# Kernel optimization log

Measured on AMD Instinct MI355X. Metric: run time of the kernel, lower is better.

The kernel has to match this reference:

```python
import jax, jax.numpy as jnp
import numpy as np

L, H, P = 16384, 1024, 512
DT_MIN, DT_MAX = 1e-3, 1e-1


def setup_inputs() -> dict:
    key = jax.random.key(0)
    ks = jax.random.split(key, 9)
    input_sequence = jax.random.normal(ks[0], (L, H), dtype=jnp.float32)
    # HiPPO-like diagonal init: negative real parts, spread imaginary parts
    Lambda_re = -0.5 * jnp.ones((P,), dtype=jnp.float32)
    Lambda_im = jnp.pi * jnp.arange(P, dtype=jnp.float32)
    # B_tilde = Vinv @ B with lecun_normal B -> ~N(0, 1/H) entries
    B_re = jax.random.normal(ks[1], (P, H), dtype=jnp.float32) / np.float32(np.sqrt(H))
    B_im = jax.random.normal(ks[2], (P, H), dtype=jnp.float32) / np.float32(np.sqrt(H))
    # C_tilde = C @ V, lecun_normal scale ~1/sqrt(2P)
    C_re = jax.random.normal(ks[3], (H, P), dtype=jnp.float32) / np.float32(np.sqrt(2 * P))
    C_im = jax.random.normal(ks[4], (H, P), dtype=jnp.float32) / np.float32(np.sqrt(2 * P))
    D = jax.random.normal(ks[5], (H,), dtype=jnp.float32)
    # log_step ~ U[log(dt_min), log(dt_max)], shape (P, 1)
    u01 = jax.random.uniform(ks[6], (P, 1), dtype=jnp.float32)
    log_step = jnp.log(DT_MIN) + u01 * (jnp.log(DT_MAX) - jnp.log(DT_MIN))
    return {
        "input_sequence": input_sequence,
        "Lambda_re": Lambda_re, "Lambda_im": Lambda_im,
        "B_re": B_re, "B_im": B_im,
        "C_re": C_re, "C_im": C_im,
        "D": D, "log_step": log_step,
    }


def _binop(q_i, q_j):
    # diagonal linear recurrence combine: x_j = A_j * x_i + b_j
    A_i, b_i = q_i
    A_j, b_j = q_j
    return (A_j * A_i, A_j * b_i + b_j)


def reference(input_sequence, Lambda_re, Lambda_im, B_re, B_im, C_re, C_im, D, log_step):
    # step_rescale = 1.0, clip_eigs = False, conj_sym = True, zoh discretization
    step = jnp.exp(log_step[:, 0])                      # (P,)
    Lam = Lambda_re + 1j * Lambda_im                    # (P,) complex64
    Lambda_bar = jnp.exp(Lam * step)                    # (P,)
    B_tilde = B_re + 1j * B_im                          # (P, H)
    B_bar = ((Lambda_bar - 1.0) / Lam)[:, None] * B_tilde  # (P, H)

    # bf16-split complex matvec: Bu_t = B_bar @ u_t (u real) for all t at once
    Bre_bf = jnp.real(B_bar).astype(jnp.bfloat16)
    Bim_bf = jnp.imag(B_bar).astype(jnp.bfloat16)
    u_bf = input_sequence.astype(jnp.bfloat16)          # (L, H)
    Bu_re = jnp.einsum('ph,lh->lp', Bre_bf, u_bf).astype(jnp.float32)
    Bu_im = jnp.einsum('ph,lh->lp', Bim_bf, u_bf).astype(jnp.float32)
    Bu = Bu_re + 1j * Bu_im                             # (L, P) complex64

    Lambda_elems = Lambda_bar * jnp.ones((input_sequence.shape[0], Lambda_bar.shape[0]),
                                         dtype=Lambda_bar.dtype)  # (L, P)
    _, xs = jax.lax.associative_scan(_binop, (Lambda_elems, Bu))  # xs: (L, P) complex64

    # bf16-split complex matvec y = C_tilde @ x, keep real part only
    Cre_bf = C_re.astype(jnp.bfloat16)
    Cim_bf = C_im.astype(jnp.bfloat16)
    xre_bf = jnp.real(xs).astype(jnp.bfloat16)
    xim_bf = jnp.imag(xs).astype(jnp.bfloat16)
    rr = jnp.einsum('hp,lp->lh', Cre_bf, xre_bf)
    ii = jnp.einsum('hp,lp->lh', Cim_bf, xim_bf)
    y_real = (rr - ii).astype(jnp.float32)              # (L, H)
    ys = 2.0 * y_real                                   # conj_sym doubling

    # feedthrough
    return ys + D * input_sequence
```

## Files before the change

### kernel.cpp

```cpp
#include <hip/hip_runtime.h>
#include <stdint.h>
#include <stddef.h>

#define L_SEQ 16384
#define H_DIM 1024
#define P_DIM 512
#define N2P   1024
#define CHUNK 64
#define NCH   256

typedef __bf16 bf16x8 __attribute__((ext_vector_type(8)));
typedef float  f32x4  __attribute__((ext_vector_type(4)));
typedef unsigned short u16x8 __attribute__((ext_vector_type(8)));

__device__ __forceinline__ unsigned short f2bf(float x) {
  unsigned int u = __float_as_uint(x);
  u += 0x7FFFu + ((u >> 16) & 1u);
  return (unsigned short)(u >> 16);
}
__device__ __forceinline__ float bf2f(unsigned short x) {
  return __uint_as_float((unsigned int)x << 16);
}

__global__ void k_prep_p(const float* __restrict__ Lre, const float* __restrict__ Lim,
                         const float* __restrict__ lstep,
                         float2* __restrict__ lam, double2* __restrict__ lamK,
                         float2* __restrict__ coeff) {
  int p = blockIdx.x * blockDim.x + threadIdx.x;
  if (p >= P_DIM) return;
  double step = exp((double)lstep[p]);
  double ar = (double)Lre[p] * step;
  double ai = (double)Lim[p] * step;
  double er = exp(ar);
  double lr = er * cos(ai), li = er * sin(ai);
  lam[p] = make_float2((float)lr, (float)li);
  double ka = (double)CHUNK * ai;
  double kr = exp((double)CHUNK * ar);
  lamK[p] = make_double2(kr * cos(ka), kr * sin(ka));
  double nr = lr - 1.0, ni = li;
  double dr = (double)Lre[p], di = (double)Lim[p];
  double den = dr * dr + di * di;
  coeff[p] = make_float2((float)((nr * dr + ni * di) / den),
                         (float)((ni * dr - nr * di) / den));
}

__global__ void k_pack_B(const float* __restrict__ Bre, const float* __restrict__ Bim,
                         const float2* __restrict__ coeff, unsigned short* __restrict__ Bp) {
  int idx = blockIdx.x * 256 + threadIdx.x;
  int p = idx >> 10, h = idx & 1023;
  float2 c = coeff[p];
  float br = Bre[idx], bi = Bim[idx];
  Bp[(size_t)(2 * p) * H_DIM + h]     = f2bf(c.x * br - c.y * bi);
  Bp[(size_t)(2 * p + 1) * H_DIM + h] = f2bf(c.x * bi + c.y * br);
}

__global__ void k_pack_C(const float* __restrict__ Cre, const float* __restrict__ Cim,
                         unsigned short* __restrict__ Cp) {
  int idx = blockIdx.x * 256 + threadIdx.x;
  int h = idx >> 10, j = idx & 1023;
  int p = j >> 1;
  float v = (j & 1) ? -Cim[(size_t)h * P_DIM + p] : Cre[(size_t)h * P_DIM + p];
  Cp[idx] = f2bf(v);
}

__global__ void k_cast_u(const float* __restrict__ U, unsigned short* __restrict__ Ub) {
  size_t base = ((size_t)blockIdx.x * 256 + threadIdx.x) * 8;
  const float4* s = (const float4*)(U + base);
  float4 v0 = s[0], v1 = s[1];
  u16x8 o;
  o[0] = f2bf(v0.x); o[1] = f2bf(v0.y); o[2] = f2bf(v0.z); o[3] = f2bf(v0.w);
  o[4] = f2bf(v1.x); o[5] = f2bf(v1.y); o[6] = f2bf(v1.z); o[7] = f2bf(v1.w);
  *(u16x8*)(Ub + base) = o;
}

template <int OUT>
__global__ void gemm_bt(const unsigned short* __restrict__ A,
                        const unsigned short* __restrict__ B,
                        void* __restrict__ Cout,
                        const unsigned short* __restrict__ Ub,
                        const float* __restrict__ Dv) {
  const int K = 1024, N = 1024;
  __shared__ unsigned short sA[128 * 64];
  __shared__ unsigned short sB[128 * 64];
  const int tid = threadIdx.x;
  const int wave = tid >> 6, lane = tid & 63;
  const int quad = lane >> 4, l16 = lane & 15;
  const int m0 = blockIdx.x * 128, n0 = blockIdx.y * 128;
  const int wm = (wave & 1) * 64, wn = (wave >> 1) * 64;

  f32x4 acc[4][4] = {};

  for (int kt = 0; kt < K; kt += 64) {
    __syncthreads();
#pragma unroll
    for (int r = 0; r < 4; ++r) {
      int id2 = r * 256 + tid;
      const unsigned short* ga = A + (size_t)(m0 + (id2 >> 3)) * K + kt + (id2 & 7) * 8;
      const unsigned short* gb = B + (size_t)(n0 + (id2 >> 3)) * K + kt + (id2 & 7) * 8;
      __builtin_amdgcn_global_load_lds(
          (const __attribute__((address_space(1))) unsigned int*)ga,
          (__attribute__((address_space(3))) unsigned int*)(sA + (r * 256 + wave * 64) * 8),
          16, 0, 0);
      __builtin_amdgcn_global_load_lds(
          (const __attribute__((address_space(1))) unsigned int*)gb,
          (__attribute__((address_space(3))) unsigned int*)(sB + (r * 256 + wave * 64) * 8),
          16, 0, 0);
    }
    __syncthreads();

#pragma unroll
    for (int h = 0; h < 2; ++h) {
      bf16x8 af[4], bfr[4];
#pragma unroll
      for (int i = 0; i < 4; ++i)
        af[i] = *(const bf16x8*)(sA + (wm + i * 16 + l16) * 64 + h * 32 + quad * 8);
#pragma unroll
      for (int j = 0; j < 4; ++j)
        bfr[j] = *(const bf16x8*)(sB + (wn + j * 16 + l16) * 64 + h * 32 + quad * 8);
#pragma unroll
      for (int i = 0; i < 4; ++i)
#pragma unroll
        for (int j = 0; j < 4; ++j)
          acc[i][j] = __builtin_amdgcn_mfma_f32_16x16x32_bf16(af[i], bfr[j], acc[i][j], 0, 0, 0);
    }
  }

#pragma unroll
  for (int i = 0; i < 4; ++i) {
#pragma unroll
    for (int j = 0; j < 4; ++j) {
      int col = n0 + wn + j * 16 + l16;
#pragma unroll
      for (int r = 0; r < 4; ++r) {
        int row = m0 + wm + i * 16 + quad * 4 + r;
        size_t o = (size_t)row * N + col;
        float v = acc[i][j][r];
        if (OUT) {
          float u = bf2f(Ub[o]);
          ((float*)Cout)[o] = 2.0f * v + Dv[col] * u;
        } else {
          ((unsigned short*)Cout)[o] = f2bf(v);
        }
      }
    }
  }
}

__global__ void k_scanA(const unsigned short* __restrict__ Bu, const float2* __restrict__ lam,
                        float2* __restrict__ csum) {
  int idx = blockIdx.x * 256 + threadIdx.x;
  int p = idx & (P_DIM - 1), chunk = idx >> 9;
  float2 l = lam[p];
  float xr = 0.f, xi = 0.f;
  const unsigned int* base = (const unsigned int*)(Bu + (size_t)chunk * CHUNK * N2P + 2 * p);
#pragma unroll 8
  for (int t = 0; t < CHUNK; ++t) {
    unsigned int v = base[(size_t)t * (N2P / 2)];
    float br = bf2f((unsigned short)(v & 0xffffu));
    float bi = bf2f((unsigned short)(v >> 16));
    float nr = fmaf(l.x, xr, fmaf(-l.y, xi, br));
    float ni = fmaf(l.x, xi, fmaf(l.y, xr, bi));
    xr = nr; xi = ni;
  }
  csum[(size_t)chunk * P_DIM + p] = make_float2(xr, xi);
}

__global__ void k_scanB(const float2* __restrict__ csum, const double2* __restrict__ lamK,
                        float2* __restrict__ carry) {
  int p = blockIdx.x * 256 + threadIdx.x;
  if (p >= P_DIM) return;
  double lkr = lamK[p].x, lki = lamK[p].y;
  double cr = 0.0, ci = 0.0;
  for (int j = 0; j < NCH; ++j) {
    carry[(size_t)j * P_DIM + p] = make_float2((float)cr, (float)ci);
    float2 s = csum[(size_t)j * P_DIM + p];
    double nr = lkr * cr - lki * ci + (double)s.x;
    double ni = lkr * ci + lki * cr + (double)s.y;
    cr = nr; ci = ni;
  }
}

__global__ void k_scanC(const unsigned short* __restrict__ Bu, const float2* __restrict__ lam,
                        const float2* __restrict__ carry, unsigned short* __restrict__ xs) {
  int idx = blockIdx.x * 256 + threadIdx.x;
  int p = idx & (P_DIM - 1), chunk = idx >> 9;
  float2 l = lam[p];
  float2 c0 = carry[(size_t)chunk * P_DIM + p];
  float xr = c0.x, xi = c0.y;
  const unsigned int* base = (const unsigned int*)(Bu + (size_t)chunk * CHUNK * N2P + 2 * p);
  unsigned int* obase = (unsigned int*)(xs + (size_t)chunk * CHUNK * N2P + 2 * p);
#pragma unroll 8
  for (int t = 0; t < CHUNK; ++t) {
    unsigned int v = base[(size_t)t * (N2P / 2)];
    float br = bf2f((unsigned short)(v & 0xffffu));
    float bi = bf2f((unsigned short)(v >> 16));
    float nr = fmaf(l.x, xr, fmaf(-l.y, xi, br));
    float ni = fmaf(l.x, xi, fmaf(l.y, xr, bi));
    xr = nr; xi = ni;
    obase[(size_t)t * (N2P / 2)] = (unsigned int)f2bf(xr) | ((unsigned int)f2bf(xi) << 16);
  }
}

extern "C" void kernel_launch(void* const* d_in, const int* in_sizes, int n_in,
                              void* d_out, int out_size, void* d_ws, size_t ws_size,
                              hipStream_t stream) {
  const float* U    = (const float*)d_in[0];
  const float* Lre  = (const float*)d_in[1];
  const float* Lim  = (const float*)d_in[2];
  const float* Bre  = (const float*)d_in[3];
  const float* Bim  = (const float*)d_in[4];
  const float* Cre  = (const float*)d_in[5];
  const float* Cim  = (const float*)d_in[6];
  const float* Dv   = (const float*)d_in[7];
  const float* lstp = (const float*)d_in[8];
  float* out = (float*)d_out;

  size_t off = 0;
  char* ws = (char*)d_ws;
  auto give = [&](size_t bytes) -> void* {
    void* p = ws + off;
    off += (bytes + 255) & ~(size_t)255;
    return p;
  };

  unsigned short* ubf  = (unsigned short*)give((size_t)L_SEQ * H_DIM * 2);
  unsigned short* Bp   = (unsigned short*)give((size_t)N2P * H_DIM * 2);
  unsigned short* Cp   = (unsigned short*)give((size_t)H_DIM * N2P * 2);
  unsigned short* Bu   = (unsigned short*)give((size_t)L_SEQ * N2P * 2);
  unsigned short* xs   = (unsigned short*)give((size_t)L_SEQ * N2P * 2);
  float2*         lam  = (float2*)give(P_DIM * sizeof(float2));
  double2*        lamK = (double2*)give(P_DIM * sizeof(double2));
  float2*         coef = (float2*)give(P_DIM * sizeof(float2));
  float2*         csum = (float2*)give((size_t)NCH * P_DIM * sizeof(float2));
  float2*         carry= (float2*)give((size_t)NCH * P_DIM * sizeof(float2));

  k_prep_p<<<2, 256, 0, stream>>>(Lre, Lim, lstp, lam, lamK, coef);
  k_pack_B<<<(P_DIM * H_DIM) / 256, 256, 0, stream>>>(Bre, Bim, coef, Bp);
  k_pack_C<<<(H_DIM * N2P) / 256, 256, 0, stream>>>(Cre, Cim, Cp);
  k_cast_u<<<(L_SEQ * H_DIM) / (256 * 8), 256, 0, stream>>>(U, ubf);

  gemm_bt<0><<<dim3(L_SEQ / 128, N2P / 128), 256, 0, stream>>>(ubf, Bp, Bu, nullptr, nullptr);

  k_scanA<<<(NCH * P_DIM) / 256, 256, 0, stream>>>(Bu, lam, csum);
  k_scanB<<<2, 256, 0, stream>>>(csum, lamK, carry);
  k_scanC<<<(NCH * P_DIM) / 256, 256, 0, stream>>>(Bu, lam, carry, xs);

  gemm_bt<1><<<dim3(L_SEQ / 128, N2P / 128), 256, 0, stream>>>(xs, Cp, out, ubf, Dv);
}
```

Measured before the change: 276.0 us.

## Fuse prep kernels, swizzle GEMM LDS layout, fold carry scan into scanC

Merges the four setup kernels (lambda prep, B pack, C pack, input cast) into one launch, recomputing the discretization coefficients per B element so no separate prep pass is needed. Applies an XOR swizzle to the GEMM shared-memory tiles to cut LDS bank conflicts on fragment reads. Removes the serial single-block carry scan: each scanC thread now recomputes its own chunk carry by walking all preceding chunk sums in fp32. That redundant per-thread loop adds up to 256 iterations of work for late chunks and drops the double-precision carry accumulation, which may lose some accuracy.

```diff
diff --git a/kernel.cpp b/kernel.cpp
--- a/kernel.cpp
+++ b/kernel.cpp
@@ -9,6 +9,11 @@
 #define CHUNK 64
 #define NCH   256
 
+#define NB_U 8192
+#define NB_B 2048
+#define NB_C 4096
+#define NB_T 2
+
 typedef __bf16 bf16x8 __attribute__((ext_vector_type(8)));
 typedef float  f32x4  __attribute__((ext_vector_type(4)));
 typedef unsigned short u16x8 __attribute__((ext_vector_type(8)));
@@ -22,55 +27,55 @@
   return __uint_as_float((unsigned int)x << 16);
 }
 
-__global__ void k_prep_p(const float* __restrict__ Lre, const float* __restrict__ Lim,
-                         const float* __restrict__ lstep,
-                         float2* __restrict__ lam, double2* __restrict__ lamK,
-                         float2* __restrict__ coeff) {
-  int p = blockIdx.x * blockDim.x + threadIdx.x;
-  if (p >= P_DIM) return;
-  double step = exp((double)lstep[p]);
-  double ar = (double)Lre[p] * step;
-  double ai = (double)Lim[p] * step;
-  double er = exp(ar);
-  double lr = er * cos(ai), li = er * sin(ai);
-  lam[p] = make_float2((float)lr, (float)li);
-  double ka = (double)CHUNK * ai;
-  double kr = exp((double)CHUNK * ar);
-  lamK[p] = make_double2(kr * cos(ka), kr * sin(ka));
-  double nr = lr - 1.0, ni = li;
-  double dr = (double)Lre[p], di = (double)Lim[p];
-  double den = dr * dr + di * di;
-  coeff[p] = make_float2((float)((nr * dr + ni * di) / den),
-                         (float)((ni * dr - nr * di) / den));
-}
-
-__global__ void k_pack_B(const float* __restrict__ Bre, const float* __restrict__ Bim,
-                         const float2* __restrict__ coeff, unsigned short* __restrict__ Bp) {
-  int idx = blockIdx.x * 256 + threadIdx.x;
-  int p = idx >> 10, h = idx & 1023;
-  float2 c = coeff[p];
-  float br = Bre[idx], bi = Bim[idx];
-  Bp[(size_t)(2 * p) * H_DIM + h]     = f2bf(c.x * br - c.y * bi);
-  Bp[(size_t)(2 * p + 1) * H_DIM + h] = f2bf(c.x * bi + c.y * br);
-}
-
-__global__ void k_pack_C(const float* __restrict__ Cre, const float* __restrict__ Cim,
-                         unsigned short* __restrict__ Cp) {
-  int idx = blockIdx.x * 256 + threadIdx.x;
-  int h = idx >> 10, j = idx & 1023;
-  int p = j >> 1;
-  float v = (j & 1) ? -Cim[(size_t)h * P_DIM + p] : Cre[(size_t)h * P_DIM + p];
-  Cp[idx] = f2bf(v);
-}
-
-__global__ void k_cast_u(const float* __restrict__ U, unsigned short* __restrict__ Ub) {
-  size_t base = ((size_t)blockIdx.x * 256 + threadIdx.x) * 8;
-  const float4* s = (const float4*)(U + base);
-  float4 v0 = s[0], v1 = s[1];
-  u16x8 o;
-  o[0] = f2bf(v0.x); o[1] = f2bf(v0.y); o[2] = f2bf(v0.z); o[3] = f2bf(v0.w);
-  o[4] = f2bf(v1.x); o[5] = f2bf(v1.y); o[6] = f2bf(v1.z); o[7] = f2bf(v1.w);
-  *(u16x8*)(Ub + base) = o;
+__global__ void k_pack_all(const float* __restrict__ U, unsigned short* __restrict__ Ub,
+                           const float* __restrict__ Bre, const float* __restrict__ Bim,
+                           unsigned short* __restrict__ Bp,
+                           const float* __restrict__ Cre, const float* __restrict__ Cim,
+                           unsigned short* __restrict__ Cp,
+                           const float* __restrict__ Lre, const float* __restrict__ Lim,
+                           const float* __restrict__ lstep,
+                           float2* __restrict__ lam, float2* __restrict__ lamK) {
+  int bid = blockIdx.x, tid = threadIdx.x;
+  if (bid < NB_U) {
+    size_t base = ((size_t)bid * 256 + tid) * 8;
+    const float4* s = (const float4*)(U + base);
+    float4 v0 = s[0], v1 = s[1];
+    u16x8 o;
+    o[0] = f2bf(v0.x); o[1] = f2bf(v0.y); o[2] = f2bf(v0.z); o[3] = f2bf(v0.w);
+    o[4] = f2bf(v1.x); o[5] = f2bf(v1.y); o[6] = f2bf(v1.z); o[7] = f2bf(v1.w);
+    *(u16x8*)(Ub + base) = o;
+  } else if (bid < NB_U + NB_B) {
+    int idx = (bid - NB_U) * 256 + tid;
+    int p = idx >> 10, h = idx & 1023;
+    double step = exp((double)lstep[p]);
+    double ar = (double)Lre[p] * step, ai = (double)Lim[p] * step;
+    double er = exp(ar);
+    double lr = er * cos(ai), li = er * sin(ai);
+    double nr = lr - 1.0, ni = li;
+    double dr = (double)Lre[p], di = (double)Lim[p];
+    double den = dr * dr + di * di;
+    float cx = (float)((nr * dr + ni * di) / den);
+    float cy = (float)((ni * dr - nr * di) / den);
+    float br = Bre[idx], bi = Bim[idx];
+    Bp[(size_t)(2 * p) * H_DIM + h]     = f2bf(cx * br - cy * bi);
+    Bp[(size_t)(2 * p + 1) * H_DIM + h] = f2bf(cx * bi + cy * br);
+  } else if (bid < NB_U + NB_B + NB_C) {
+    int idx = (bid - NB_U - NB_B) * 256 + tid;
+    int h = idx >> 10, j = idx & 1023;
+    int p = j >> 1;
+    float v = (j & 1) ? -Cim[(size_t)h * P_DIM + p] : Cre[(size_t)h * P_DIM + p];
+    Cp[idx] = f2bf(v);
+  } else {
+    int p = (bid - NB_U - NB_B - NB_C) * 256 + tid;
+    if (p < P_DIM) {
+      double step = exp((double)lstep[p]);
+      double ar = (double)Lre[p] * step, ai = (double)Lim[p] * step;
+      double er = exp(ar);
+      lam[p] = make_float2((float)(er * cos(ai)), (float)(er * sin(ai)));
+      double ka = (double)CHUNK * ai, kr = exp((double)CHUNK * ar);
+      lamK[p] = make_float2((float)(kr * cos(ka)), (float)(kr * sin(ka)));
+    }
+  }
 }
 
 template <int OUT>
@@ -94,9 +99,11 @@
     __syncthreads();
 #pragma unroll
     for (int r = 0; r < 4; ++r) {
-      int id2 = r * 256 + tid;
-      const unsigned short* ga = A + (size_t)(m0 + (id2 >> 3)) * K + kt + (id2 & 7) * 8;
-      const unsigned short* gb = B + (size_t)(n0 + (id2 >> 3)) * K + kt + (id2 & 7) * 8;
+      int s = r * 256 + tid;
+      int row = s >> 3;
+      int j8 = (s & 7) ^ (row & 7);
+      const unsigned short* ga = A + (size_t)(m0 + row) * K + kt + j8 * 8;
+      const unsigned short* gb = B + (size_t)(n0 + row) * K + kt + j8 * 8;
       __builtin_amdgcn_global_load_lds(
           (const __attribute__((address_space(1))) unsigned int*)ga,
           (__attribute__((address_space(3))) unsigned int*)(sA + (r * 256 + wave * 64) * 8),
@@ -112,11 +119,15 @@
     for (int h = 0; h < 2; ++h) {
       bf16x8 af[4], bfr[4];
 #pragma unroll
-      for (int i = 0; i < 4; ++i)
-        af[i] = *(const bf16x8*)(sA + (wm + i * 16 + l16) * 64 + h * 32 + quad * 8);
-#pragma unroll
-      for (int j = 0; j < 4; ++j)
-        bfr[j] = *(const bf16x8*)(sB + (wn + j * 16 + l16) * 64 + h * 32 + quad * 8);
+      for (int i = 0; i < 4; ++i) {
+        int ra = wm + i * 16 + l16;
+        af[i] = *(const bf16x8*)(sA + ra * 64 + (((h << 2) + quad) ^ (ra & 7)) * 8);
+      }
+#pragma unroll
+      for (int j = 0; j < 4; ++j) {
+        int rb = wn + j * 16 + l16;
+        bfr[j] = *(const bf16x8*)(sB + rb * 64 + (((h << 2) + quad) ^ (rb & 7)) * 8);
+      }
 #pragma unroll
       for (int i = 0; i < 4; ++i)
 #pragma unroll
@@ -165,28 +176,22 @@
   csum[(size_t)chunk * P_DIM + p] = make_float2(xr, xi);
 }
 
-__global__ void k_scanB(const float2* __restrict__ csum, const double2* __restrict__ lamK,
-                        float2* __restrict__ carry) {
-  int p = blockIdx.x * 256 + threadIdx.x;
-  if (p >= P_DIM) return;
-  double lkr = lamK[p].x, lki = lamK[p].y;
-  double cr = 0.0, ci = 0.0;
-  for (int j = 0; j < NCH; ++j) {
-    carry[(size_t)j * P_DIM + p] = make_float2((float)cr, (float)ci);
-    float2 s = csum[(size_t)j * P_DIM + p];
-    double nr = lkr * cr - lki * ci + (double)s.x;
-    double ni = lkr * ci + lki * cr + (double)s.y;
-    cr = nr; ci = ni;
-  }
-}
-
 __global__ void k_scanC(const unsigned short* __restrict__ Bu, const float2* __restrict__ lam,
-                        const float2* __restrict__ carry, unsigned short* __restrict__ xs) {
+                        const float2* __restrict__ lamK, const float2* __restrict__ csum,
+                        unsigned short* __restrict__ xs) {
   int idx = blockIdx.x * 256 + threadIdx.x;
   int p = idx & (P_DIM - 1), chunk = idx >> 9;
   float2 l = lam[p];
-  float2 c0 = carry[(size_t)chunk * P_DIM + p];
-  float xr = c0.x, xi = c0.y;
+  float2 lk = lamK[p];
+  float cr = 0.f, ci = 0.f;
+#pragma unroll 4
+  for (int j = 0; j < chunk; ++j) {
+    float2 s = csum[(size_t)j * P_DIM + p];
+    float nr = fmaf(lk.x, cr, fmaf(-lk.y, ci, s.x));
+    float ni = fmaf(lk.x, ci, fmaf(lk.y, cr, s.y));
+    cr = nr; ci = ni;
+  }
+  float xr = cr, xi = ci;
   const unsigned int* base = (const unsigned int*)(Bu + (size_t)chunk * CHUNK * N2P + 2 * p);
   unsigned int* obase = (unsigned int*)(xs + (size_t)chunk * CHUNK * N2P + 2 * p);
 #pragma unroll 8
@@ -229,21 +234,16 @@
   unsigned short* Bu   = (unsigned short*)give((size_t)L_SEQ * N2P * 2);
   unsigned short* xs   = (unsigned short*)give((size_t)L_SEQ * N2P * 2);
   float2*         lam  = (float2*)give(P_DIM * sizeof(float2));
-  double2*        lamK = (double2*)give(P_DIM * sizeof(double2));
-  float2*         coef = (float2*)give(P_DIM * sizeof(float2));
+  float2*         lamK = (float2*)give(P_DIM * sizeof(float2));
   float2*         csum = (float2*)give((size_t)NCH * P_DIM * sizeof(float2));
-  float2*         carry= (float2*)give((size_t)NCH * P_DIM * sizeof(float2));
-
-  k_prep_p<<<2, 256, 0, stream>>>(Lre, Lim, lstp, lam, lamK, coef);
-  k_pack_B<<<(P_DIM * H_DIM) / 256, 256, 0, stream>>>(Bre, Bim, coef, Bp);
-  k_pack_C<<<(H_DIM * N2P) / 256, 256, 0, stream>>>(Cre, Cim, Cp);
-  k_cast_u<<<(L_SEQ * H_DIM) / (256 * 8), 256, 0, stream>>>(U, ubf);
+
+  k_pack_all<<<NB_U + NB_B + NB_C + NB_T, 256, 0, stream>>>(
+      U, ubf, Bre, Bim, Bp, Cre, Cim, Cp, Lre, Lim, lstp, lam, lamK);
 
   gemm_bt<0><<<dim3(L_SEQ / 128, N2P / 128), 256, 0, stream>>>(ubf, Bp, Bu, nullptr, nullptr);
 
   k_scanA<<<(NCH * P_DIM) / 256, 256, 0, stream>>>(Bu, lam, csum);
-  k_scanB<<<2, 256, 0, stream>>>(csum, lamK, carry);
-  k_scanC<<<(NCH * P_DIM) / 256, 256, 0, stream>>>(Bu, lam, carry, xs);
+  k_scanC<<<(NCH * P_DIM) / 256, 256, 0, stream>>>(Bu, lam, lamK, csum, xs);
 
   gemm_bt<1><<<dim3(L_SEQ / 128, N2P / 128), 256, 0, stream>>>(xs, Cp, out, ubf, Dv);
 }
```

Measured after the change: 270.6 us. -2.0%, faster.
